# Kernel optimization log

Hardware: AMD Instinct MI355X
Metric: run time of the kernel (lower is better)

Reference implementation:

```python
import jax, jax.numpy as jnp
import numpy as np

F_NODES = 360        # nodes per graph == num_features (square connectome)
NUM_GRAPHS = 128
NUM_EDGES = 1_000_000
C = 128              # hidden_channels
NUM_LAYERS = 3
HIDDEN = 512
NUM_CLASSES = 2
EPS = 1e-5


def _bn(x, g, b):
    # BatchNorm1d in training mode: biased batch statistics over the batch dim.
    m = x.mean(axis=0)
    v = x.var(axis=0)
    return (x - m) * jax.lax.rsqrt(v + EPS) * g + b


def _gcn(x, W, b, src, dst):
    # GCNConv: x' = D^{-1/2} (A + I) D^{-1/2} (x W) + b
    N = x.shape[0]
    h = x @ W                                   # [N, C]
    loop = jnp.arange(N, dtype=src.dtype)
    src2 = jnp.concatenate([src, loop])
    dst2 = jnp.concatenate([dst, loop])
    deg = jax.ops.segment_sum(jnp.ones_like(dst2, dtype=h.dtype), dst2, num_segments=N)
    dinv = jnp.where(deg > 0, jax.lax.rsqrt(deg), 0.0)
    norm = dinv[src2] * dinv[dst2]              # [E+N]
    out = jax.ops.segment_sum(h[src2] * norm[:, None], dst2, num_segments=N)
    return out + b


def setup_inputs() -> dict:
    key = jax.random.key(0)
    ks = jax.random.split(key, 16)
    N = NUM_GRAPHS * F_NODES
    x = jax.random.normal(ks[0], (N, F_NODES), jnp.float32)
    # edges confined within each graph
    g = jax.random.randint(ks[1], (NUM_EDGES,), 0, NUM_GRAPHS)
    edge_src = g * F_NODES + jax.random.randint(ks[2], (NUM_EDGES,), 0, F_NODES)
    edge_dst = g * F_NODES + jax.random.randint(ks[3], (NUM_EDGES,), 0, F_NODES)
    batch = jnp.repeat(jnp.arange(NUM_GRAPHS), F_NODES)

    def lin(k, fi, fo):
        s = 1.0 / np.sqrt(fi)
        return jax.random.uniform(k, (fi, fo), jnp.float32, -s, s)

    input_dim = F_NODES * (F_NODES + 1) // 2    # 64980
    input_dim1 = input_dim + C * NUM_LAYERS     # 65364
    H2 = HIDDEN // 2
    params = dict(
        Wc1=lin(ks[4], F_NODES, C), bc1=jnp.zeros((C,), jnp.float32),
        Wc2=lin(ks[5], C, C), bc2=jnp.zeros((C,), jnp.float32),
        Wc3=lin(ks[6], C, C), bc3=jnp.zeros((C,), jnp.float32),
        bn_g=jnp.ones((input_dim,), jnp.float32), bn_b=jnp.zeros((input_dim,), jnp.float32),
        bnh_g=jnp.ones((C * NUM_LAYERS,), jnp.float32), bnh_b=jnp.zeros((C * NUM_LAYERS,), jnp.float32),
        W1=lin(ks[7], input_dim1, HIDDEN), b1=jnp.zeros((HIDDEN,), jnp.float32),
        g1=jnp.ones((HIDDEN,), jnp.float32), be1=jnp.zeros((HIDDEN,), jnp.float32),
        W2=lin(ks[8], HIDDEN, H2), b2=jnp.zeros((H2,), jnp.float32),
        g2=jnp.ones((H2,), jnp.float32), be2=jnp.zeros((H2,), jnp.float32),
        W3=lin(ks[9], H2, H2), b3=jnp.zeros((H2,), jnp.float32),
        g3=jnp.ones((H2,), jnp.float32), be3=jnp.zeros((H2,), jnp.float32),
        W4=lin(ks[10], H2, NUM_CLASSES), b4=jnp.zeros((NUM_CLASSES,), jnp.float32),
    )
    return {"x": x, "edge_src": edge_src, "edge_dst": edge_dst, "batch": batch, **params}


def reference(x, edge_src, edge_dst, batch,
              Wc1, bc1, Wc2, bc2, Wc3, bc3,
              bn_g, bn_b, bnh_g, bnh_b,
              W1, b1, g1, be1, W2, b2, g2, be2, W3, b3, g3, be3, W4, b4):
    N, F = x.shape
    B = N // F                                   # nodes per graph == F
    # stacked GCN convs with tanh
    xs = [x]
    for W, b in ((Wc1, bc1), (Wc2, bc2), (Wc3, bc3)):
        xs.append(jnp.tanh(_gcn(xs[-1], W, b, edge_src, edge_dst)))
    # per-graph upper-triangular gather of the raw connectome (vectorized)
    iu0, iu1 = np.triu_indices(F)
    x0 = xs[0].reshape(B, F, F)[:, iu0, iu1]     # [B, F(F+1)/2]
    x0 = _bn(x0, bn_g, bn_b)
    # per-layer segment-mean pooling over graphs
    cnt = jax.ops.segment_sum(jnp.ones((N,), x.dtype), batch, num_segments=B)
    h = jnp.concatenate(
        [jax.ops.segment_sum(xx, batch, num_segments=B) / cnt[:, None] for xx in xs[1:]],
        axis=1)                                  # [B, C*num_layers]
    h = _bn(h, bnh_g, bnh_b)
    z = jnp.concatenate([x0, h], axis=1)         # [B, input_dim1]
    # MLP head (dropout in eval mode => identity)
    z = jax.nn.relu(_bn(z @ W1 + b1, g1, be1))
    z = jax.nn.relu(_bn(z @ W2 + b2, g2, be2))
    z = jax.nn.relu(_bn(z @ W3 + b3, g3, be3))
    return jax.nn.log_softmax(z @ W4 + b4, axis=1)
```

## Files before the change

### kernel.cpp

```cpp
#include <hip/hip_runtime.h>
#include <hip/hip_bf16.h>
#include <math.h>

#define FN 360
#define NG 128
#define NN 46080
#define CH 128
#define NE 1000000
#define TRI 64980
#define D1 65364
#define ZLD 65376
#define H1 512
#define H2 256
#define EPS 1e-5f
#define NSPLIT 64
#define NB1 720
#define ERNG 4096
#define NR 245
#define NCH 8
#define CROWS 45
#define BCAP 8
#define OVCAP 192
#define OVGCAP 32768
#define NAGG 384

typedef unsigned short u16;
typedef __attribute__((ext_vector_type(8))) short bf16x8;
typedef __attribute__((ext_vector_type(4))) float f32x4;

__device__ __forceinline__ float bf2f(u16 v) {
  union { unsigned u; float f; } x; x.u = ((unsigned)v) << 16; return x.f;
}
__device__ __forceinline__ u16 f2bf(float f) {
  union { float f; unsigned u; } x; x.f = f;
  unsigned r = x.u + 0x7fffu + ((x.u >> 16) & 1u);
  return (u16)(r >> 16);
}
__device__ __forceinline__ bf16x8 bzero8() {
  bf16x8 z;
#pragma unroll
  for (int j = 0; j < 8; j++) z[j] = 0;
  return z;
}

static const size_t Z_OFF    = 0;
static const size_t PART_OFF = 16736256;
static const size_t EBUF_OFF = PART_OFF;
static const size_t CNT_OFF  = PART_OFF + 4014080;
static const size_t OVF_OFF  = CNT_OFF + 1003520;
static const size_t Y1_OFF   = 50290688;
static const size_t A1_OFF   = 50552832;
static const size_t A2_OFF   = 50683904;
static const size_t A3_OFF   = 50749440;
static const size_t DEG_OFF  = 66355200;
static const size_t HP_OFF   = 66539520;
static const size_t OVN_OFF  = 66736128;
static const size_t AB_OFF   = 66740224;
static const size_t PT_OFF   = 99917824;
static const size_t H_OFF    = 111714304;

__device__ __forceinline__ void pt_epilogue(
    u16 (*PST)[72], const f32x4 (*acc)[4], u16* __restrict__ PT,
    int m0blk, int wid, int quad, int l16) {
  int n0w = (wid >> 1) * 64;
  int mh = (wid & 1) * 32;
#pragma unroll
  for (int tm = 0; tm < 2; tm++)
#pragma unroll
    for (int tn = 0; tn < 4; tn++) {
      int col = n0w + tn * 16 + l16;
#pragma unroll
      for (int r = 0; r < 4; r++)
        PST[col][mh + tm * 16 + quad * 4 + r] = f2bf(acc[tm][tn][r]);
    }
  __syncthreads();
  int t = threadIdx.x;
  int col = t >> 1, seg = t & 1;
#pragma unroll
  for (int u = 0; u < 4; u++) {
    int lrl = seg * 32 + u * 8;
    int row = m0blk + lrl;
    int g = row / FN, lr = row - g * FN;
    *(bf16x8*)(PT + ((size_t)g * CH + col) * FN + lr) = *(const bf16x8*)&PST[col][lrl];
  }
}

__global__ __launch_bounds__(256) void k_bucket(
    const int* __restrict__ src, const int* __restrict__ dst,
    float* __restrict__ deg, u16* __restrict__ ebuf, int* __restrict__ cnt,
    int* __restrict__ govn, unsigned* __restrict__ govf) {
  __shared__ int cur[NG * NCH];
  __shared__ u16 bins[NG * NCH][BCAP];
  __shared__ unsigned ovf[OVCAP];
  __shared__ int ovn, obase;
  int r = blockIdx.x;
  for (int i = threadIdx.x; i < NG * NCH; i += 256) cur[i] = 0;
  if (threadIdx.x == 0) ovn = 0;
  __syncthreads();
  int base = r * ERNG;
#pragma unroll 4
  for (int it = 0; it < ERNG / 256; it++) {
    int e = base + it * 256 + threadIdx.x;
    if (e < NE) {
      int s = src[e], d = dst[e];
      atomicAdd(&deg[d], 1.0f);
      int g = d / FN;
      int ls = s - g * FN, ld = d - g * FN;
      int ch = ld / CROWS;
      int gc = g * NCH + ch;
      int slot = atomicAdd(&cur[gc], 1);
      if (slot < BCAP) {
        bins[gc][slot] = (u16)(ls | ((ld - ch * CROWS) << 9));
      } else {
        int o = atomicAdd(&ovn, 1);
        if (o < OVCAP) ovf[o] = (unsigned)ls | ((unsigned)ld << 9) | ((unsigned)g << 18);
      }
    }
  }
  __syncthreads();
  {
    const f32x4* sb = (const f32x4*)bins;
    f32x4* gb = (f32x4*)(ebuf + (size_t)r * (NG * NCH) * BCAP);
    for (int i = threadIdx.x; i < NG * NCH * BCAP / 8; i += 256) gb[i] = sb[i];
  }
  for (int i = threadIdx.x; i < NG * NCH; i += 256) {
    int c = cur[i];
    cnt[r * (NG * NCH) + i] = c < BCAP ? c : BCAP;
  }
  if (threadIdx.x == 0) {
    int n = ovn < OVCAP ? ovn : OVCAP;
    obase = atomicAdd(govn, n);
  }
  __syncthreads();
  int n = ovn < OVCAP ? ovn : OVCAP;
  for (int i = threadIdx.x; i < n; i += 256)
    if (obase + i < OVGCAP) govf[obase + i] = ovf[i];
}

__global__ __launch_bounds__(256) void k_gemm1(
    const float* __restrict__ X, const float* __restrict__ W,
    u16* __restrict__ PT) {
  __shared__ __attribute__((aligned(16))) union { u16 WT[128][40]; u16 PST[128][72]; } sh;
  const int K = FN;
  int wid = threadIdx.x >> 6, lane = threadIdx.x & 63;
  int quad = lane >> 4, l16 = lane & 15;
  int m0blk = blockIdx.x * 64;
  int m0 = m0blk + (wid & 1) * 32;
  int n0w = (wid >> 1) * 64;
  int kl = threadIdx.x >> 3, nseg = (threadIdx.x & 7) * 16;
  f32x4 acc[2][4];
#pragma unroll
  for (int i = 0; i < 2; i++)
#pragma unroll
    for (int j = 0; j < 4; j++) acc[i][j] = (f32x4){0,0,0,0};
  for (int k0 = 0; k0 < K; k0 += 32) {
    __syncthreads();
    int kg = k0 + kl;
    if (kg < K) {
      const float* wrow = W + (size_t)kg * CH + nseg;
      f32x4 w0 = *(const f32x4*)(wrow);
      f32x4 w1 = *(const f32x4*)(wrow + 4);
      f32x4 w2 = *(const f32x4*)(wrow + 8);
      f32x4 w3 = *(const f32x4*)(wrow + 12);
#pragma unroll
      for (int j = 0; j < 4; j++) {
        sh.WT[nseg + j][kl]      = f2bf(w0[j]);
        sh.WT[nseg + 4 + j][kl]  = f2bf(w1[j]);
        sh.WT[nseg + 8 + j][kl]  = f2bf(w2[j]);
        sh.WT[nseg + 12 + j][kl] = f2bf(w3[j]);
      }
    } else {
#pragma unroll
      for (int j = 0; j < 16; j++) sh.WT[nseg + j][kl] = 0;
    }
    __syncthreads();
    int kk = k0 + quad * 8;
    bool kin = kk < K;
    bf16x8 af[2];
#pragma unroll
    for (int tm = 0; tm < 2; tm++) {
      int row = m0 + tm * 16 + l16;
      bf16x8 a = bzero8();
      if (kin) {
        f32x4 va = *(const f32x4*)(X + (size_t)row * K + kk);
        f32x4 vb = *(const f32x4*)(X + (size_t)row * K + kk + 4);
#pragma unroll
        for (int j = 0; j < 4; j++) { a[j] = (short)f2bf(va[j]); a[4 + j] = (short)f2bf(vb[j]); }
      }
      af[tm] = a;
    }
    bf16x8 bfr[4];
#pragma unroll
    for (int tn = 0; tn < 4; tn++)
      bfr[tn] = *(const bf16x8*)&sh.WT[n0w + tn * 16 + l16][quad * 8];
#pragma unroll
    for (int tm = 0; tm < 2; tm++)
#pragma unroll
      for (int tn = 0; tn < 4; tn++)
        acc[tm][tn] = __builtin_amdgcn_mfma_f32_16x16x32_bf16(af[tm], bfr[tn], acc[tm][tn], 0, 0, 0);
  }
  __syncthreads();
  pt_epilogue(sh.PST, acc, PT, m0blk, wid, quad, l16);
}

__global__ __launch_bounds__(256) void k_abuild3(
    const u16* __restrict__ ebuf, const int* __restrict__ cnt,
    const int* __restrict__ govn, const unsigned* __restrict__ govf,
    const float* __restrict__ deg, u16* __restrict__ Ab) {
  __shared__ __attribute__((aligned(16))) float sA[CROWS * FN];
  __shared__ float sdg[FN];
  __shared__ int scnt[NR];
  int g = blockIdx.x >> 3, ch = blockIdx.x & 7;
  int gc = g * NCH + ch;
  int r0 = ch * CROWS;
  for (int i = threadIdx.x; i < CROWS * FN / 4; i += 256) ((f32x4*)sA)[i] = (f32x4){0,0,0,0};
  for (int i = threadIdx.x; i < FN; i += 256) sdg[i] = rsqrtf(deg[g * FN + i] + 1.0f);
  for (int i = threadIdx.x; i < NR; i += 256) scnt[i] = cnt[i * (NG * NCH) + gc];
  __syncthreads();
  for (int idx = threadIdx.x; idx < NR * BCAP; idx += 256) {
    int r = idx >> 3, sl = idx & (BCAP - 1);
    if (sl < scnt[r]) {
      u16 p = ebuf[((size_t)r * (NG * NCH) + gc) * BCAP + sl];
      int ls = p & 511, ldr = (p >> 9) & 63;
      atomicAdd(&sA[ldr * FN + ls], sdg[ls] * sdg[r0 + ldr]);
    }
  }
  int on = *govn; if (on > OVGCAP) on = OVGCAP;
  for (int i = threadIdx.x; i < on; i += 256) {
    unsigned p = govf[i];
    if ((int)(p >> 18) == g) {
      int ld = (p >> 9) & 511, lr = ld - r0;
      if ((unsigned)lr < (unsigned)CROWS) {
        int ls = p & 511;
        atomicAdd(&sA[lr * FN + ls], sdg[ls] * sdg[ld]);
      }
    }
  }
  __syncthreads();
  if (threadIdx.x < CROWS) {
    int l = r0 + threadIdx.x;
    float dv = sdg[l];
    sA[threadIdx.x * FN + l] += dv * dv;
  }
  __syncthreads();
  unsigned* dstu = (unsigned*)(Ab + (size_t)g * FN * FN + (size_t)r0 * FN);
  for (int i = threadIdx.x; i < CROWS * FN / 2; i += 256) {
    unsigned lo = f2bf(sA[2 * i]), hi = f2bf(sA[2 * i + 1]);
    dstu[i] = lo | (hi << 16);
  }
}

template<bool GUARD>
__device__ __forceinline__ void gbig_body(
    const u16* __restrict__ Z, const float* __restrict__ W1f,
    float* __restrict__ part, int s, int n0b) {
  __shared__ __attribute__((aligned(16))) u16 WT[128][40];
  int wid = threadIdx.x >> 6, lane = threadIdx.x & 63;
  int quad = lane >> 4, l16 = lane & 15;
  int m0 = wid * 32;
  int kl = threadIdx.x >> 3, nseg = (threadIdx.x & 7) * 16;
  int kbeg = s * 1024;
  int kend = GUARD ? ((ZLD < kbeg + 1024) ? ZLD : (kbeg + 1024)) : (kbeg + 1024);
  f32x4 acc[2][8];
#pragma unroll
  for (int i = 0; i < 2; i++)
#pragma unroll
    for (int j = 0; j < 8; j++) acc[i][j] = (f32x4){0,0,0,0};
  for (int k0 = kbeg; k0 < kend; k0 += 32) {
    __syncthreads();
    int kg = k0 + kl;
    if (!GUARD || kg < D1) {
      const float* wrow = W1f + (size_t)kg * H1 + n0b + nseg;
      f32x4 w0 = *(const f32x4*)(wrow);
      f32x4 w1 = *(const f32x4*)(wrow + 4);
      f32x4 w2 = *(const f32x4*)(wrow + 8);
      f32x4 w3 = *(const f32x4*)(wrow + 12);
#pragma unroll
      for (int j = 0; j < 4; j++) {
        WT[nseg + j][kl]      = f2bf(w0[j]);
        WT[nseg + 4 + j][kl]  = f2bf(w1[j]);
        WT[nseg + 8 + j][kl]  = f2bf(w2[j]);
        WT[nseg + 12 + j][kl] = f2bf(w3[j]);
      }
    } else {
#pragma unroll
      for (int j = 0; j < 16; j++) WT[nseg + j][kl] = 0;
    }
    __syncthreads();
    int kk = k0 + quad * 8;
    bf16x8 af[2];
#pragma unroll
    for (int tm = 0; tm < 2; tm++) {
      int row = m0 + tm * 16 + l16;
      af[tm] = *(const bf16x8*)(Z + (size_t)row * ZLD + kk);
    }
    bf16x8 bfr[8];
#pragma unroll
    for (int tn = 0; tn < 8; tn++)
      bfr[tn] = *(const bf16x8*)&WT[tn * 16 + l16][quad * 8];
#pragma unroll
    for (int tm = 0; tm < 2; tm++)
#pragma unroll
      for (int tn = 0; tn < 8; tn++)
        acc[tm][tn] = __builtin_amdgcn_mfma_f32_16x16x32_bf16(af[tm], bfr[tn], acc[tm][tn], 0, 0, 0);
  }
#pragma unroll
  for (int tm = 0; tm < 2; tm++)
#pragma unroll
    for (int tn = 0; tn < 8; tn++) {
      int col = n0b + tn * 16 + l16;
      int rowb = m0 + tm * 16 + quad * 4;
#pragma unroll
      for (int r = 0; r < 4; r++)
        part[((size_t)s * NG + rowb + r) * H1 + col] = acc[tm][tn][r];
    }
}

__global__ __launch_bounds__(256) void k_agg(
    const u16* __restrict__ Ab, const u16* __restrict__ PT,
    const float* __restrict__ bias, u16* __restrict__ Hout,
    float* __restrict__ hp, int loff,
    const u16* __restrict__ Z, const float* __restrict__ W1f,
    float* __restrict__ part) {
  if (blockIdx.x >= NAGG) {
    int id2 = blockIdx.x - NAGG;
    gbig_body<false>(Z, W1f, part, id2 >> 2, (id2 & 3) * 128);
    return;
  }
  __shared__ __attribute__((aligned(16))) u16 sA[128][40];
  __shared__ __attribute__((aligned(16))) u16 sP[128][40];
  __shared__ float ps[8][128];
  int id = blockIdx.x;
  int g = (id & 7) + 8 * (id / 24);
  int mb = (id % 24) >> 3;
  int m0blk = mb * 128;
  int wid = threadIdx.x >> 6, lane = threadIdx.x & 63;
  int quad = lane >> 4, l16 = lane & 15;
  int mw = (wid & 1) * 64, nw = (wid >> 1) * 64;
  const u16* Abg = Ab + (size_t)g * FN * FN;
  const u16* PTg = PT + (size_t)g * CH * FN;
  int t = threadIdx.x;
  f32x4 acc[4][4];
#pragma unroll
  for (int i = 0; i < 4; i++)
#pragma unroll
    for (int j = 0; j < 4; j++) acc[i][j] = (f32x4){0,0,0,0};
  bf16x8 ra[2], rp[2];
#define AGG_LOAD(k0)                                                          \
  {                                                                           \
    _Pragma("unroll")                                                         \
    for (int i = 0; i < 2; i++) {                                             \
      int lin = i * 256 + t;                                                  \
      int row = lin >> 2, q = lin & 3;                                        \
      int kg = (k0) + q * 8;                                                  \
      int grow = m0blk + row;                                                 \
      ra[i] = (kg < FN && grow < FN)                                          \
                  ? *(const bf16x8*)(Abg + (size_t)grow * FN + kg) : bzero8();\
      rp[i] = (kg < FN)                                                       \
                  ? *(const bf16x8*)(PTg + (size_t)row * FN + kg) : bzero8(); \
    }                                                                         \
  }
  AGG_LOAD(0)
  for (int step = 0; step < 12; step++) {
    __syncthreads();
#pragma unroll
    for (int i = 0; i < 2; i++) {
      int lin = i * 256 + t;
      int row = lin >> 2, q = lin & 3;
      *(bf16x8*)&sA[row][q * 8] = ra[i];
      *(bf16x8*)&sP[row][q * 8] = rp[i];
    }
    __syncthreads();
    if (step < 11) AGG_LOAD((step + 1) * 32)
    bf16x8 af[4], bp[4];
#pragma unroll
    for (int tm = 0; tm < 4; tm++)
      af[tm] = *(const bf16x8*)&sA[mw + tm * 16 + l16][quad * 8];
#pragma unroll
    for (int tn = 0; tn < 4; tn++)
      bp[tn] = *(const bf16x8*)&sP[nw + tn * 16 + l16][quad * 8];
#pragma unroll
    for (int tm = 0; tm < 4; tm++)
#pragma unroll
      for (int tn = 0; tn < 4; tn++)
        acc[tm][tn] = __builtin_amdgcn_mfma_f32_16x16x32_bf16(af[tm], bp[tn], acc[tm][tn], 0, 0, 0);
  }
#undef AGG_LOAD
  float lsum[4] = {0.f, 0.f, 0.f, 0.f};
#pragma unroll
  for (int tm = 0; tm < 4; tm++)
#pragma unroll
    for (int tn = 0; tn < 4; tn++) {
      int col = nw + tn * 16 + l16;
      float bc = bias[col];
      int rowb = m0blk + mw + tm * 16 + quad * 4;
#pragma unroll
      for (int r = 0; r < 4; r++) {
        int row = rowb + r;
        if (row < FN) {
          float tt = tanhf(acc[tm][tn][r] + bc);
          if (Hout) Hout[(size_t)(g * FN + row) * CH + col] = f2bf(tt);
          lsum[tn] += tt;
        }
      }
    }
  int cid = (wid & 1) * 4 + quad;
#pragma unroll
  for (int tn = 0; tn < 4; tn++) ps[cid][nw + tn * 16 + l16] = lsum[tn];
  __syncthreads();
  if (threadIdx.x < 128) {
    float s = 0.f;
#pragma unroll
    for (int c = 0; c < 8; c++) s += ps[c][threadIdx.x];
    atomicAdd(&hp[g * 384 + loff + threadIdx.x], s);
  }
}

__global__ __launch_bounds__(256) void k_gemm_xw_bf16(
    const u16* __restrict__ X, const float* __restrict__ W,
    u16* __restrict__ PT) {
  __shared__ __attribute__((aligned(16))) union { u16 WT[128][40]; u16 PST[128][72]; } sh;
  int wid = threadIdx.x >> 6, lane = threadIdx.x & 63;
  int quad = lane >> 4, l16 = lane & 15;
  int m0blk = blockIdx.x * 64;
  int m0 = m0blk + (wid & 1) * 32;
  int n0w = (wid >> 1) * 64;
  int kl = threadIdx.x >> 3, nseg = (threadIdx.x & 7) * 16;
  f32x4 acc[2][4];
#pragma unroll
  for (int i = 0; i < 2; i++)
#pragma unroll
    for (int j = 0; j < 4; j++) acc[i][j] = (f32x4){0,0,0,0};
  for (int k0 = 0; k0 < CH; k0 += 32) {
    __syncthreads();
    int kg = k0 + kl;
    const float* wrow = W + (size_t)kg * CH + nseg;
    f32x4 w0 = *(const f32x4*)(wrow);
    f32x4 w1 = *(const f32x4*)(wrow + 4);
    f32x4 w2 = *(const f32x4*)(wrow + 8);
    f32x4 w3 = *(const f32x4*)(wrow + 12);
#pragma unroll
    for (int j = 0; j < 4; j++) {
      sh.WT[nseg + j][kl]      = f2bf(w0[j]);
      sh.WT[nseg + 4 + j][kl]  = f2bf(w1[j]);
      sh.WT[nseg + 8 + j][kl]  = f2bf(w2[j]);
      sh.WT[nseg + 12 + j][kl] = f2bf(w3[j]);
    }
    __syncthreads();
    int kk = k0 + quad * 8;
    bf16x8 af[2];
#pragma unroll
    for (int tm = 0; tm < 2; tm++) {
      int row = m0 + tm * 16 + l16;
      af[tm] = *(const bf16x8*)(X + (size_t)row * CH + kk);
    }
    bf16x8 bfr[4];
#pragma unroll
    for (int tn = 0; tn < 4; tn++)
      bfr[tn] = *(const bf16x8*)&sh.WT[n0w + tn * 16 + l16][quad * 8];
#pragma unroll
    for (int tm = 0; tm < 2; tm++)
#pragma unroll
      for (int tn = 0; tn < 4; tn++)
        acc[tm][tn] = __builtin_amdgcn_mfma_f32_16x16x32_bf16(af[tm], bfr[tn], acc[tm][tn], 0, 0, 0);
  }
  __syncthreads();
  pt_epilogue(sh.PST, acc, PT, m0blk, wid, quad, l16);
}

__global__ __launch_bounds__(256) void k_gemm2tri(
    const u16* __restrict__ X, const float* __restrict__ W,
    u16* __restrict__ PT,
    const float* __restrict__ x, const float* __restrict__ gam,
    const float* __restrict__ bet, u16* __restrict__ z) {
  if (blockIdx.x >= NB1) {
    int i = blockIdx.x - NB1;
    int off = i * FN - (i * (i - 1)) / 2;
    for (int j = i + (int)threadIdx.x; j < FN; j += 256) {
      float s = 0.f, ss = 0.f;
#pragma unroll 8
      for (int b = 0; b < NG; b++) {
        float v = x[(size_t)(b * FN + i) * FN + j];
        s += v; ss += v * v;
      }
      float mean = s * (1.0f / NG);
      float var = fmaxf(ss * (1.0f / NG) - mean * mean, 0.f);
      float rstd = rsqrtf(var + EPS);
      int f = off + (j - i);
      float ga = gam[f] * rstd;
      float bb = bet[f] - mean * ga;
#pragma unroll 8
      for (int b = 0; b < NG; b++) {
        float v = x[(size_t)(b * FN + i) * FN + j];
        z[(size_t)b * ZLD + f] = f2bf(v * ga + bb);
      }
    }
    return;
  }
  __shared__ __attribute__((aligned(16))) union { u16 WT[128][40]; u16 PST[128][72]; } sh;
  int wid = threadIdx.x >> 6, lane = threadIdx.x & 63;
  int quad = lane >> 4, l16 = lane & 15;
  int m0blk = blockIdx.x * 64;
  int m0 = m0blk + (wid & 1) * 32;
  int n0w = (wid >> 1) * 64;
  int kl = threadIdx.x >> 3, nseg = (threadIdx.x & 7) * 16;
  f32x4 acc[2][4];
#pragma unroll
  for (int i = 0; i < 2; i++)
#pragma unroll
    for (int j = 0; j < 4; j++) acc[i][j] = (f32x4){0,0,0,0};
  for (int k0 = 0; k0 < CH; k0 += 32) {
    __syncthreads();
    int kg = k0 + kl;
    const float* wrow = W + (size_t)kg * CH + nseg;
    f32x4 w0 = *(const f32x4*)(wrow);
    f32x4 w1 = *(const f32x4*)(wrow + 4);
    f32x4 w2 = *(const f32x4*)(wrow + 8);
    f32x4 w3 = *(const f32x4*)(wrow + 12);
#pragma unroll
    for (int j = 0; j < 4; j++) {
      sh.WT[nseg + j][kl]      = f2bf(w0[j]);
      sh.WT[nseg + 4 + j][kl]  = f2bf(w1[j]);
      sh.WT[nseg + 8 + j][kl]  = f2bf(w2[j]);
      sh.WT[nseg + 12 + j][kl] = f2bf(w3[j]);
    }
    __syncthreads();
    int kk = k0 + quad * 8;
    bf16x8 af[2];
#pragma unroll
    for (int tm = 0; tm < 2; tm++) {
      int row = m0 + tm * 16 + l16;
      af[tm] = *(const bf16x8*)(X + (size_t)row * CH + kk);
    }
    bf16x8 bfr[4];
#pragma unroll
    for (int tn = 0; tn < 4; tn++)
      bfr[tn] = *(const bf16x8*)&sh.WT[n0w + tn * 16 + l16][quad * 8];
#pragma unroll
    for (int tm = 0; tm < 2; tm++)
#pragma unroll
      for (int tn = 0; tn < 4; tn++)
        acc[tm][tn] = __builtin_amdgcn_mfma_f32_16x16x32_bf16(af[tm], bfr[tn], acc[tm][tn], 0, 0, 0);
  }
  __syncthreads();
  pt_epilogue(sh.PST, acc, PT, m0blk, wid, quad, l16);
}

__global__ void k_hpbn(const float* __restrict__ hp,
                       const float* __restrict__ hgam, const float* __restrict__ hbet,
                       u16* __restrict__ z) {
  for (int c = threadIdx.x; c < 384; c += 256) {
    float s = 0.f, ss = 0.f;
#pragma unroll 8
    for (int m = 0; m < NG; m++) {
      float v = hp[m * 384 + c] * (1.0f / FN);
      s += v; ss += v * v;
    }
    float mean = s * (1.0f / NG);
    float var = fmaxf(ss * (1.0f / NG) - mean * mean, 0.f);
    float rstd = rsqrtf(var + EPS);
    float ga = hgam[c] * rstd;
    float bb = hbet[c] - mean * ga;
#pragma unroll 8
    for (int m = 0; m < NG; m++)
      z[(size_t)m * ZLD + TRI + c] = f2bf(hp[m * 384 + c] * (1.0f / FN) * ga + bb);
  }
  if (threadIdx.x < NG) {
    for (int t = 0; t < ZLD - D1; t++)
      z[(size_t)threadIdx.x * ZLD + D1 + t] = 0;
  }
}

__global__ __launch_bounds__(256) void k_gbig_tail(
    const u16* __restrict__ Z, const float* __restrict__ W1f, float* __restrict__ part) {
  gbig_body<true>(Z, W1f, part, NSPLIT - 1, blockIdx.x * 128);
}

__global__ void k_red(const float* __restrict__ part, float* __restrict__ y1) {
  int idx = blockIdx.x * 256 + threadIdx.x;
  float s = 0.f;
#pragma unroll 8
  for (int i = 0; i < NSPLIT; i++) s += part[(size_t)i * 65536 + idx];
  y1[idx] = s;
}

__global__ __launch_bounds__(256) void k_bnrelu(
    const float* __restrict__ y, const float* __restrict__ gam,
    const float* __restrict__ bet, u16* __restrict__ a, int N) {
  __shared__ float sb[4][64], sb2[4][64];
  int c63 = threadIdx.x & 63;
  int grp = threadIdx.x >> 6;
  int c = blockIdx.x * 64 + c63;
  float s = 0.f, ss = 0.f;
#pragma unroll 8
  for (int m = grp * 32; m < grp * 32 + 32; m++) {
    float v = y[(size_t)m * N + c]; s += v; ss += v * v;
  }
  sb[grp][c63] = s; sb2[grp][c63] = ss;
  __syncthreads();
  float S = sb[0][c63] + sb[1][c63] + sb[2][c63] + sb[3][c63];
  float SS = sb2[0][c63] + sb2[1][c63] + sb2[2][c63] + sb2[3][c63];
  float mean = S * (1.0f / NG);
  float var = fmaxf(SS * (1.0f / NG) - mean * mean, 0.f);
  float rstd = rsqrtf(var + EPS);
  float ga = gam[c] * rstd;
  float bb = bet[c] - mean * ga;
#pragma unroll 8
  for (int m = grp * 32; m < grp * 32 + 32; m++) {
    float v = y[(size_t)m * N + c] * ga + bb;
    a[(size_t)m * N + c] = f2bf(fmaxf(v, 0.f));
  }
}

__global__ __launch_bounds__(256) void k_mlpbn(
    const u16* __restrict__ A, const float* __restrict__ W,
    const float* __restrict__ gam, const float* __restrict__ bet,
    u16* __restrict__ aout, int K, int N) {
  __shared__ __attribute__((aligned(16))) u16 WT[64][40];
  __shared__ float rs[4][4][4][16], rss[4][4][4][16];
  int wid = threadIdx.x >> 6, lane = threadIdx.x & 63;
  int quad = lane >> 4, l16 = lane & 15;
  int n0b = blockIdx.x * 64;
  int m0 = wid * 32;
  int kl = threadIdx.x >> 3;
  int nseg = (threadIdx.x & 7) * 8;
  f32x4 acc[2][4];
#pragma unroll
  for (int i = 0; i < 2; i++)
#pragma unroll
    for (int j = 0; j < 4; j++) acc[i][j] = (f32x4){0,0,0,0};
  for (int k0 = 0; k0 < K; k0 += 32) {
    __syncthreads();
    const float* wrow = W + (size_t)(k0 + kl) * N + n0b + nseg;
    f32x4 w0 = *(const f32x4*)(wrow);
    f32x4 w1 = *(const f32x4*)(wrow + 4);
#pragma unroll
    for (int j = 0; j < 4; j++) {
      WT[nseg + j][kl]     = f2bf(w0[j]);
      WT[nseg + 4 + j][kl] = f2bf(w1[j]);
    }
    __syncthreads();
    int kk = k0 + quad * 8;
    bf16x8 af[2];
#pragma unroll
    for (int tm = 0; tm < 2; tm++) {
      int row = m0 + tm * 16 + l16;
      af[tm] = *(const bf16x8*)(A + (size_t)row * K + kk);
    }
    bf16x8 bfr[4];
#pragma unroll
    for (int tn = 0; tn < 4; tn++)
      bfr[tn] = *(const bf16x8*)&WT[tn * 16 + l16][quad * 8];
#pragma unroll
    for (int tm = 0; tm < 2; tm++)
#pragma unroll
      for (int tn = 0; tn < 4; tn++)
        acc[tm][tn] = __builtin_amdgcn_mfma_f32_16x16x32_bf16(af[tm], bfr[tn], acc[tm][tn], 0, 0, 0);
  }
  __syncthreads();
#pragma unroll
  for (int tn = 0; tn < 4; tn++) {
    float s = 0.f, ss = 0.f;
#pragma unroll
    for (int tm = 0; tm < 2; tm++)
#pragma unroll
      for (int r = 0; r < 4; r++) { float v = acc[tm][tn][r]; s += v; ss += v * v; }
    rs[wid][quad][tn][l16] = s;
    rss[wid][quad][tn][l16] = ss;
  }
  __syncthreads();
#pragma unroll
  for (int tn = 0; tn < 4; tn++) {
    float S = 0.f, SS = 0.f;
#pragma unroll
    for (int w = 0; w < 4; w++)
#pragma unroll
      for (int q = 0; q < 4; q++) { S += rs[w][q][tn][l16]; SS += rss[w][q][tn][l16]; }
    float mean = S * (1.0f / NG);
    float var = fmaxf(SS * (1.0f / NG) - mean * mean, 0.f);
    float rstd = rsqrtf(var + EPS);
    int col = n0b + tn * 16 + l16;
    float ga = gam[col] * rstd;
    float bb = bet[col] - mean * ga;
#pragma unroll
    for (int tm = 0; tm < 2; tm++) {
      int rowb = m0 + tm * 16 + quad * 4;
#pragma unroll
      for (int r = 0; r < 4; r++) {
        float v = acc[tm][tn][r] * ga + bb;
        aout[(size_t)(rowb + r) * N + col] = f2bf(fmaxf(v, 0.f));
      }
    }
  }
}

__global__ void k_head(const u16* __restrict__ a3, const float* __restrict__ W4,
                       const float* __restrict__ b4, float* __restrict__ out) {
  __shared__ float w4s[H2 * 2];
  int m = threadIdx.x;
  for (int i = m; i < H2 * 2; i += 128) w4s[i] = W4[i];
  __syncthreads();
  float a0 = b4[0], a1 = b4[1];
  for (int k0 = 0; k0 < H2; k0 += 8) {
    bf16x8 v = *(const bf16x8*)(a3 + (size_t)m * H2 + k0);
#pragma unroll
    for (int j = 0; j < 8; j++) {
      float f = bf2f((u16)v[j]);
      a0 += f * w4s[(k0 + j) * 2];
      a1 += f * w4s[(k0 + j) * 2 + 1];
    }
  }
  float mx = fmaxf(a0, a1);
  float lse = mx + logf(expf(a0 - mx) + expf(a1 - mx));
  out[m * 2]     = a0 - lse;
  out[m * 2 + 1] = a1 - lse;
}

extern "C" void kernel_launch(void* const* d_in, const int* in_sizes, int n_in,
                              void* d_out, int out_size, void* d_ws, size_t ws_size,
                              hipStream_t stream) {
  const float* x    = (const float*)d_in[0];
  const int* esrc   = (const int*)d_in[1];
  const int* edst   = (const int*)d_in[2];
  const float* Wc1 = (const float*)d_in[4];  const float* bc1 = (const float*)d_in[5];
  const float* Wc2 = (const float*)d_in[6];  const float* bc2 = (const float*)d_in[7];
  const float* Wc3 = (const float*)d_in[8];  const float* bc3 = (const float*)d_in[9];
  const float* bn_g = (const float*)d_in[10]; const float* bn_b = (const float*)d_in[11];
  const float* bnh_g = (const float*)d_in[12]; const float* bnh_b = (const float*)d_in[13];
  const float* W1 = (const float*)d_in[14];
  const float* g1 = (const float*)d_in[16]; const float* be1 = (const float*)d_in[17];
  const float* W2 = (const float*)d_in[18];
  const float* g2 = (const float*)d_in[20]; const float* be2 = (const float*)d_in[21];
  const float* W3 = (const float*)d_in[22];
  const float* g3 = (const float*)d_in[24]; const float* be3 = (const float*)d_in[25];
  const float* W4 = (const float*)d_in[26]; const float* b4 = (const float*)d_in[27];

  char* ws = (char*)d_ws;
  float* deg  = (float*)(ws + DEG_OFF);
  float* hp   = (float*)(ws + HP_OFF);
  int*   govn = (int*)(ws + OVN_OFF);
  u16*   Ab   = (u16*)(ws + AB_OFF);
  u16*   ebuf = (u16*)(ws + EBUF_OFF);
  int*   cnt  = (int*)(ws + CNT_OFF);
  unsigned* govf = (unsigned*)(ws + OVF_OFF);
  u16*   PT   = (u16*)(ws + PT_OFF);
  u16*   h    = (u16*)(ws + H_OFF);
  u16*   z    = (u16*)(ws + Z_OFF);
  float* part = (float*)(ws + PART_OFF);
  float* y1   = (float*)(ws + Y1_OFF);
  u16*   a1   = (u16*)(ws + A1_OFF);
  u16*   a2   = (u16*)(ws + A2_OFF);
  u16*   a3   = (u16*)(ws + A3_OFF);

  (void)hipMemsetAsync(deg, 0, (size_t)NN * 4 + (size_t)NG * 384 * 4 + 4, stream);

  dim3 b256(256);
  k_bucket<<<dim3(NR), b256, 0, stream>>>(esrc, edst, deg, ebuf, cnt, govn, govf);
  k_gemm1<<<dim3(NB1), b256, 0, stream>>>(x, Wc1, PT);
  k_abuild3<<<dim3(NG * NCH), b256, 0, stream>>>(ebuf, cnt, govn, govf, deg, Ab);
  k_agg<<<dim3(NAGG), b256, 0, stream>>>(Ab, PT, bc1, h, hp, 0, z, W1, part);
  k_gemm2tri<<<dim3(NB1 + FN), b256, 0, stream>>>(h, Wc2, PT, x, bn_g, bn_b, z);
  k_agg<<<dim3(NAGG + 252), b256, 0, stream>>>(Ab, PT, bc2, h, hp, CH, z, W1, part);
  k_gemm_xw_bf16<<<dim3(NB1), b256, 0, stream>>>(h, Wc3, PT);
  k_agg<<<dim3(NAGG), b256, 0, stream>>>(Ab, PT, bc3, (u16*)nullptr, hp, 2 * CH, z, W1, part);
  k_hpbn<<<dim3(1), b256, 0, stream>>>(hp, bnh_g, bnh_b, z);
  k_gbig_tail<<<dim3(4), b256, 0, stream>>>(z, W1, part);
  k_red<<<dim3(65536 / 256), b256, 0, stream>>>(part, y1);
  k_bnrelu<<<dim3(H1 / 64), b256, 0, stream>>>(y1, g1, be1, a1, H1);
  k_mlpbn<<<dim3(H2 / 64), b256, 0, stream>>>(a1, W2, g2, be2, a2, H1, H2);
  k_mlpbn<<<dim3(H2 / 64), b256, 0, stream>>>(a2, W3, g3, be3, a3, H2, H2);
  k_head<<<dim3(1), dim3(128), 0, stream>>>(a3, W4, b4, (float*)d_out);
}
```

Baseline: 644.2 us.

## Fuse bucketing into gemm1, widen agg to 512 threads, move big-GEMM blocks

Merges the edge-bucketing kernel into the first XW GEMM as extra blocks, so both run in one launch and can overlap. Rewrites the aggregation kernel to use 512 threads with a 64-wide K step (6 iterations instead of 12), giving each warp a 64x32 tile. The piggybacked big W1 GEMM blocks move from the second agg launch to the third-layer XW GEMM launch. The larger K tile raises LDS use, and the reshuffled concurrency may shift load balance between the co-scheduled work.

```diff
diff --git a/kernel.cpp b/kernel.cpp
--- a/kernel.cpp
+++ b/kernel.cpp
@@ -85,62 +85,68 @@
   }
 }
 
-__global__ __launch_bounds__(256) void k_bucket(
+__global__ __launch_bounds__(256) void k_gemm1bkt(
+    const float* __restrict__ X, const float* __restrict__ W,
+    u16* __restrict__ PT,
     const int* __restrict__ src, const int* __restrict__ dst,
     float* __restrict__ deg, u16* __restrict__ ebuf, int* __restrict__ cnt,
     int* __restrict__ govn, unsigned* __restrict__ govf) {
-  __shared__ int cur[NG * NCH];
-  __shared__ u16 bins[NG * NCH][BCAP];
-  __shared__ unsigned ovf[OVCAP];
-  __shared__ int ovn, obase;
-  int r = blockIdx.x;
-  for (int i = threadIdx.x; i < NG * NCH; i += 256) cur[i] = 0;
-  if (threadIdx.x == 0) ovn = 0;
-  __syncthreads();
-  int base = r * ERNG;
+  __shared__ __attribute__((aligned(16))) union {
+    struct {
+      int cur[NG * NCH];
+      u16 bins[NG * NCH][BCAP];
+      unsigned ovf[OVCAP];
+      int ovn, obase;
+    } b;
+    u16 WT[128][40];
+    u16 PST[128][72];
+  } sh;
+  if (blockIdx.x >= NB1) {
+    int r = blockIdx.x - NB1;
+    for (int i = threadIdx.x; i < NG * NCH; i += 256) sh.b.cur[i] = 0;
+    if (threadIdx.x == 0) sh.b.ovn = 0;
+    __syncthreads();
+    int base = r * ERNG;
 #pragma unroll 4
-  for (int it = 0; it < ERNG / 256; it++) {
-    int e = base + it * 256 + threadIdx.x;
-    if (e < NE) {
-      int s = src[e], d = dst[e];
-      atomicAdd(&deg[d], 1.0f);
-      int g = d / FN;
-      int ls = s - g * FN, ld = d - g * FN;
-      int ch = ld / CROWS;
-      int gc = g * NCH + ch;
-      int slot = atomicAdd(&cur[gc], 1);
-      if (slot < BCAP) {
-        bins[gc][slot] = (u16)(ls | ((ld - ch * CROWS) << 9));
-      } else {
-        int o = atomicAdd(&ovn, 1);
-        if (o < OVCAP) ovf[o] = (unsigned)ls | ((unsigned)ld << 9) | ((unsigned)g << 18);
-      }
-    }
-  }
-  __syncthreads();
-  {
-    const f32x4* sb = (const f32x4*)bins;
-    f32x4* gb = (f32x4*)(ebuf + (size_t)r * (NG * NCH) * BCAP);
-    for (int i = threadIdx.x; i < NG * NCH * BCAP / 8; i += 256) gb[i] = sb[i];
-  }
-  for (int i = threadIdx.x; i < NG * NCH; i += 256) {
-    int c = cur[i];
-    cnt[r * (NG * NCH) + i] = c < BCAP ? c : BCAP;
-  }
-  if (threadIdx.x == 0) {
-    int n = ovn < OVCAP ? ovn : OVCAP;
-    obase = atomicAdd(govn, n);
-  }
-  __syncthreads();
-  int n = ovn < OVCAP ? ovn : OVCAP;
-  for (int i = threadIdx.x; i < n; i += 256)
-    if (obase + i < OVGCAP) govf[obase + i] = ovf[i];
-}
-
-__global__ __launch_bounds__(256) void k_gemm1(
-    const float* __restrict__ X, const float* __restrict__ W,
-    u16* __restrict__ PT) {
-  __shared__ __attribute__((aligned(16))) union { u16 WT[128][40]; u16 PST[128][72]; } sh;
+    for (int it = 0; it < ERNG / 256; it++) {
+      int e = base + it * 256 + threadIdx.x;
+      if (e < NE) {
+        int s = src[e], d = dst[e];
+        atomicAdd(&deg[d], 1.0f);
+        int g = d / FN;
+        int ls = s - g * FN, ld = d - g * FN;
+        int ch = ld / CROWS;
+        int gc = g * NCH + ch;
+        int slot = atomicAdd(&sh.b.cur[gc], 1);
+        if (slot < BCAP) {
+          sh.b.bins[gc][slot] = (u16)(ls | ((ld - ch * CROWS) << 9));
+        } else {
+          int o = atomicAdd(&sh.b.ovn, 1);
+          if (o < OVCAP) sh.b.ovf[o] = (unsigned)ls | ((unsigned)ld << 9) | ((unsigned)g << 18);
+        }
+      }
+    }
+    __syncthreads();
+    {
+      const f32x4* sb = (const f32x4*)sh.b.bins;
+      f32x4* gb = (f32x4*)(ebuf + (size_t)r * (NG * NCH) * BCAP);
+      for (int i = threadIdx.x; i < NG * NCH * BCAP / 8; i += 256) gb[i] = sb[i];
+    }
+    for (int i = threadIdx.x; i < NG * NCH; i += 256) {
+      int c = sh.b.cur[i];
+      cnt[r * (NG * NCH) + i] = c < BCAP ? c : BCAP;
+    }
+    if (threadIdx.x == 0) {
+      int n = sh.b.ovn < OVCAP ? sh.b.ovn : OVCAP;
+      sh.b.obase = atomicAdd(govn, n);
+    }
+    __syncthreads();
+    int n = sh.b.ovn < OVCAP ? sh.b.ovn : OVCAP;
+    int ob = sh.b.obase;
+    for (int i = threadIdx.x; i < n; i += 256)
+      if (ob + i < OVGCAP) govf[ob + i] = sh.b.ovf[i];
+    return;
+  }
   const int K = FN;
   int wid = threadIdx.x >> 6, lane = threadIdx.x & 63;
   int quad = lane >> 4, l16 = lane & 15;
@@ -316,42 +322,36 @@
     }
 }
 
-__global__ __launch_bounds__(256) void k_agg(
+__global__ __launch_bounds__(512) void k_agg(
     const u16* __restrict__ Ab, const u16* __restrict__ PT,
     const float* __restrict__ bias, u16* __restrict__ Hout,
-    float* __restrict__ hp, int loff,
-    const u16* __restrict__ Z, const float* __restrict__ W1f,
-    float* __restrict__ part) {
-  if (blockIdx.x >= NAGG) {
-    int id2 = blockIdx.x - NAGG;
-    gbig_body<false>(Z, W1f, part, id2 >> 2, (id2 & 3) * 128);
-    return;
-  }
-  __shared__ __attribute__((aligned(16))) u16 sA[128][40];
-  __shared__ __attribute__((aligned(16))) u16 sP[128][40];
+    float* __restrict__ hp, int loff) {
+  __shared__ __attribute__((aligned(16))) u16 sA[128][72];
+  __shared__ __attribute__((aligned(16))) u16 sP[128][72];
   __shared__ float ps[8][128];
   int id = blockIdx.x;
   int g = (id & 7) + 8 * (id / 24);
   int mb = (id % 24) >> 3;
   int m0blk = mb * 128;
-  int wid = threadIdx.x >> 6, lane = threadIdx.x & 63;
+  int t = threadIdx.x;
+  int wid = t >> 6, lane = t & 63;
   int quad = lane >> 4, l16 = lane & 15;
-  int mw = (wid & 1) * 64, nw = (wid >> 1) * 64;
+  int wr = wid & 1, wc = wid >> 1;
+  int mw = wr * 64, nw = wc * 32;
   const u16* Abg = Ab + (size_t)g * FN * FN;
   const u16* PTg = PT + (size_t)g * CH * FN;
-  int t = threadIdx.x;
-  f32x4 acc[4][4];
+  f32x4 acc[4][2];
 #pragma unroll
   for (int i = 0; i < 4; i++)
 #pragma unroll
-    for (int j = 0; j < 4; j++) acc[i][j] = (f32x4){0,0,0,0};
+    for (int j = 0; j < 2; j++) acc[i][j] = (f32x4){0,0,0,0};
   bf16x8 ra[2], rp[2];
 #define AGG_LOAD(k0)                                                          \
   {                                                                           \
     _Pragma("unroll")                                                         \
     for (int i = 0; i < 2; i++) {                                             \
-      int lin = i * 256 + t;                                                  \
-      int row = lin >> 2, q = lin & 3;                                        \
+      int lin = i * 512 + t;                                                  \
+      int row = lin >> 3, q = lin & 7;                                        \
       int kg = (k0) + q * 8;                                                  \
       int grow = m0blk + row;                                                 \
       ra[i] = (kg < FN && grow < FN)                                          \
@@ -361,36 +361,39 @@
     }                                                                         \
   }
   AGG_LOAD(0)
-  for (int step = 0; step < 12; step++) {
+  for (int step = 0; step < 6; step++) {
     __syncthreads();
 #pragma unroll
     for (int i = 0; i < 2; i++) {
-      int lin = i * 256 + t;
-      int row = lin >> 2, q = lin & 3;
+      int lin = i * 512 + t;
+      int row = lin >> 3, q = lin & 7;
       *(bf16x8*)&sA[row][q * 8] = ra[i];
       *(bf16x8*)&sP[row][q * 8] = rp[i];
     }
     __syncthreads();
-    if (step < 11) AGG_LOAD((step + 1) * 32)
-    bf16x8 af[4], bp[4];
-#pragma unroll
-    for (int tm = 0; tm < 4; tm++)
-      af[tm] = *(const bf16x8*)&sA[mw + tm * 16 + l16][quad * 8];
-#pragma unroll
-    for (int tn = 0; tn < 4; tn++)
-      bp[tn] = *(const bf16x8*)&sP[nw + tn * 16 + l16][quad * 8];
-#pragma unroll
-    for (int tm = 0; tm < 4; tm++)
-#pragma unroll
-      for (int tn = 0; tn < 4; tn++)
-        acc[tm][tn] = __builtin_amdgcn_mfma_f32_16x16x32_bf16(af[tm], bp[tn], acc[tm][tn], 0, 0, 0);
+    if (step < 5) AGG_LOAD((step + 1) * 64)
+#pragma unroll
+    for (int sub = 0; sub < 2; sub++) {
+      bf16x8 af[4], bp[2];
+#pragma unroll
+      for (int tm = 0; tm < 4; tm++)
+        af[tm] = *(const bf16x8*)&sA[mw + tm * 16 + l16][sub * 32 + quad * 8];
+#pragma unroll
+      for (int tn = 0; tn < 2; tn++)
+        bp[tn] = *(const bf16x8*)&sP[nw + tn * 16 + l16][sub * 32 + quad * 8];
+#pragma unroll
+      for (int tm = 0; tm < 4; tm++)
+#pragma unroll
+        for (int tn = 0; tn < 2; tn++)
+          acc[tm][tn] = __builtin_amdgcn_mfma_f32_16x16x32_bf16(af[tm], bp[tn], acc[tm][tn], 0, 0, 0);
+    }
   }
 #undef AGG_LOAD
-  float lsum[4] = {0.f, 0.f, 0.f, 0.f};
+  float lsum[2] = {0.f, 0.f};
 #pragma unroll
   for (int tm = 0; tm < 4; tm++)
 #pragma unroll
-    for (int tn = 0; tn < 4; tn++) {
+    for (int tn = 0; tn < 2; tn++) {
       int col = nw + tn * 16 + l16;
       float bc = bias[col];
       int rowb = m0blk + mw + tm * 16 + quad * 4;
@@ -404,21 +407,28 @@
         }
       }
     }
-  int cid = (wid & 1) * 4 + quad;
-#pragma unroll
-  for (int tn = 0; tn < 4; tn++) ps[cid][nw + tn * 16 + l16] = lsum[tn];
-  __syncthreads();
-  if (threadIdx.x < 128) {
+  int cid = wr * 4 + quad;
+#pragma unroll
+  for (int tn = 0; tn < 2; tn++) ps[cid][nw + tn * 16 + l16] = lsum[tn];
+  __syncthreads();
+  if (t < 128) {
     float s = 0.f;
 #pragma unroll
-    for (int c = 0; c < 8; c++) s += ps[c][threadIdx.x];
-    atomicAdd(&hp[g * 384 + loff + threadIdx.x], s);
+    for (int c = 0; c < 8; c++) s += ps[c][t];
+    atomicAdd(&hp[g * 384 + loff + t], s);
   }
 }
 
 __global__ __launch_bounds__(256) void k_gemm_xw_bf16(
     const u16* __restrict__ X, const float* __restrict__ W,
-    u16* __restrict__ PT) {
+    u16* __restrict__ PT,
+    const u16* __restrict__ Z, const float* __restrict__ W1f,
+    float* __restrict__ part) {
+  if (blockIdx.x >= NB1) {
+    int id2 = blockIdx.x - NB1;
+    gbig_body<false>(Z, W1f, part, id2 >> 2, (id2 & 3) * 128);
+    return;
+  }
   __shared__ __attribute__((aligned(16))) union { u16 WT[128][40]; u16 PST[128][72]; } sh;
   int wid = threadIdx.x >> 6, lane = threadIdx.x & 63;
   int quad = lane >> 4, l16 = lane & 15;
@@ -755,14 +765,14 @@
   (void)hipMemsetAsync(deg, 0, (size_t)NN * 4 + (size_t)NG * 384 * 4 + 4, stream);
 
   dim3 b256(256);
-  k_bucket<<<dim3(NR), b256, 0, stream>>>(esrc, edst, deg, ebuf, cnt, govn, govf);
-  k_gemm1<<<dim3(NB1), b256, 0, stream>>>(x, Wc1, PT);
+  dim3 b512(512);
+  k_gemm1bkt<<<dim3(NB1 + NR), b256, 0, stream>>>(x, Wc1, PT, esrc, edst, deg, ebuf, cnt, govn, govf);
   k_abuild3<<<dim3(NG * NCH), b256, 0, stream>>>(ebuf, cnt, govn, govf, deg, Ab);
-  k_agg<<<dim3(NAGG), b256, 0, stream>>>(Ab, PT, bc1, h, hp, 0, z, W1, part);
+  k_agg<<<dim3(NAGG), b512, 0, stream>>>(Ab, PT, bc1, h, hp, 0);
   k_gemm2tri<<<dim3(NB1 + FN), b256, 0, stream>>>(h, Wc2, PT, x, bn_g, bn_b, z);
-  k_agg<<<dim3(NAGG + 252), b256, 0, stream>>>(Ab, PT, bc2, h, hp, CH, z, W1, part);
-  k_gemm_xw_bf16<<<dim3(NB1), b256, 0, stream>>>(h, Wc3, PT);
-  k_agg<<<dim3(NAGG), b256, 0, stream>>>(Ab, PT, bc3, (u16*)nullptr, hp, 2 * CH, z, W1, part);
+  k_agg<<<dim3(NAGG), b512, 0, stream>>>(Ab, PT, bc2, h, hp, CH);
+  k_gemm_xw_bf16<<<dim3(NB1 + 252), b256, 0, stream>>>(h, Wc3, PT, z, W1, part);
+  k_agg<<<dim3(NAGG), b512, 0, stream>>>(Ab, PT, bc3, (u16*)nullptr, hp, 2 * CH);
   k_hpbn<<<dim3(1), b256, 0, stream>>>(hp, bnh_g, bnh_b, z);
   k_gbig_tail<<<dim3(4), b256, 0, stream>>>(z, W1, part);
   k_red<<<dim3(65536 / 256), b256, 0, stream>>>(part, y1);
```

Result: faster. 620.6 us (-3.7%).
